# Performance work log

Measured on AMD Instinct MI355X. Metric: run time of the kernel, lower is better.

## Reference

```python
import jax, jax.numpy as jnp
import numpy as np
from jax import lax


def _conv(x, w, b):
    y = lax.conv_general_dilated(x, w, (1, 1), 'VALID',
                                 dimension_numbers=('NCHW', 'OIHW', 'NCHW'))
    return y + b[None, :, None, None]


def _cubic_weights(t):
    # torch bicubic kernel, A = -0.75
    A = -0.75
    def k1(u):
        return ((A + 2.0) * u - (A + 3.0)) * u * u + 1.0
    def k2(u):
        return ((A * u - 5.0 * A) * u + 8.0 * A) * u - 4.0 * A
    return (k2(t + 1.0), k1(t), k1(1.0 - t), k2(2.0 - t))


def _grid_sample_bicubic(img, grid):
    # img: (N,C,H,W); grid: (N,H,W,2) with (x,y) in [-1,1];
    # align_corners=False, padding_mode='zeros' (torch semantics)
    N, C, H, W = img.shape
    x = ((grid[..., 0] + 1.0) * W - 1.0) * 0.5
    y = ((grid[..., 1] + 1.0) * H - 1.0) * 0.5
    x0 = jnp.floor(x)
    y0 = jnp.floor(y)
    wx = _cubic_weights(x - x0)
    wy = _cubic_weights(y - y0)
    x0i = x0.astype(jnp.int32)
    y0i = y0.astype(jnp.int32)
    flat = img.reshape(N, C, H * W)
    Ho, Wo = x.shape[1], x.shape[2]
    out = jnp.zeros((N, C, Ho, Wo), img.dtype)
    for i in range(4):
        yi = y0i - 1 + i
        vy = (yi >= 0) & (yi < H)
        yic = jnp.clip(yi, 0, H - 1)
        for j in range(4):
            xj = x0i - 1 + j
            valid = vy & (xj >= 0) & (xj < W)
            xjc = jnp.clip(xj, 0, W - 1)
            idx = (yic * W + xjc).reshape(N, 1, Ho * Wo)
            v = jnp.take_along_axis(flat, idx, axis=2).reshape(N, C, Ho, Wo)
            w = jnp.where(valid, wy[i] * wx[j], 0.0)[:, None]
            out = out + v * w
    return out


def _warp_images(disp, images, novelLocation):
    # disp: (N,1,H,W); images: (N,20,H,W); novelLocation: (N,2,H,W)
    N, _, H, W = disp.shape
    d = jnp.moveaxis(disp, 1, -1)                      # (N,H,W,1)
    us = jnp.arange(H, dtype=jnp.float32)
    vs = jnp.arange(W, dtype=jnp.float32)
    gu, gv = jnp.meshgrid(us, vs, indexing='ij')       # torch default indexing
    base = jnp.stack((gu, gv), axis=-1)[None]          # (1,H,W,2) in (row,col)
    q = jnp.moveaxis(novelLocation, 1, -1)             # (N,H,W,2)
    scale = jnp.array([H - 1, W - 1], jnp.float32)
    warped = []
    for i in range(4):
        off = 5 * i
        img = images[:, off:off + 3]
        p = jnp.moveaxis(images[:, off + 3:off + 5], 1, -1)
        loc = base + (p - q) * d                       # (N,H,W,2) (row,col)
        loc = (loc / scale - 0.5) * 2.0
        loc = loc[..., ::-1]                           # flip -> (x=col, y=row)
        warped.append(_grid_sample_bicubic(img, loc))
    return jnp.concatenate(warped + [disp, novelLocation], axis=1)  # (N,15,H,W)


def _disparity_net(x, w1, b1, w2, b2, w3, b3, w4, b4):
    x = jax.nn.relu(_conv(x, w1, b1))
    x = jax.nn.relu(_conv(x, w2, b2))
    x = jax.nn.relu(_conv(x, w3, b3))
    return _conv(x, w4, b4)


def setup_inputs() -> dict:
    key = jax.random.key(0)
    ks = jax.random.split(key, 20)
    inp = {
        'disparityFeatures': jax.random.normal(ks[0], (4, 200, 268, 268), jnp.float32),
        'colorFeatures': jax.random.normal(ks[1], (4, 22, 256, 256), jnp.float32),
    }
    def conv_p(kw, kb, o, c, k):
        fan_in = c * k * k
        w = jax.random.normal(kw, (o, c, k, k), jnp.float32) / np.sqrt(fan_in)
        b = jax.random.normal(kb, (o,), jnp.float32) * 0.01
        return w, b
    inp['dw1'], inp['db1'] = conv_p(ks[2], ks[3], 100, 200, 7)
    inp['dw2'], inp['db2'] = conv_p(ks[4], ks[5], 100, 100, 5)
    inp['dw3'], inp['db3'] = conv_p(ks[6], ks[7], 50, 100, 3)
    inp['dw4'], inp['db4'] = conv_p(ks[8], ks[9], 1, 50, 1)
    inp['cw1'], inp['cb1'] = conv_p(ks[10], ks[11], 100, 15, 7)
    inp['cw2'], inp['cb2'] = conv_p(ks[12], ks[13], 100, 100, 5)
    inp['cw3'], inp['cb3'] = conv_p(ks[14], ks[15], 50, 100, 3)
    inp['cw4'], inp['cb4'] = conv_p(ks[16], ks[17], 3, 50, 1)
    return inp


def reference(disparityFeatures, colorFeatures,
              dw1, db1, dw2, db2, dw3, db3, dw4, db4,
              cw1, cb1, cw2, cb2, cw3, cb3, cw4, cb4):
    images = colorFeatures[:, :-2]
    novelLocation = colorFeatures[:, -2:]
    disparity = _disparity_net(disparityFeatures, dw1, db1, dw2, db2, dw3, db3, dw4, db4)
    warps = _warp_images(disparity, images, novelLocation)
    finalImg = _disparity_net(warps, cw1, cb1, cw2, cb2, cw3, cb3, cw4, cb4)
    return finalImg
```

## Files before the change

### kernel.cpp

```cpp
#include <hip/hip_runtime.h>
#include <cstddef>
#include <cstdint>

typedef _Float16 f16x8 __attribute__((ext_vector_type(8)));
typedef _Float16 f16x4 __attribute__((ext_vector_type(4)));
typedef float    f32x16 __attribute__((ext_vector_type(16)));

__global__ __launch_bounds__(256) void wtrans_kernel(
    const float* __restrict__ w, _Float16* __restrict__ Bt,
    int IC, int OC, int G, int K, int R, int ksteps)
{
    int gid = blockIdx.x * 256 + threadIdx.x;
    if (gid >= ksteps * G * 64) return;
    int ks   = gid / (G * 64);
    int rr   = gid - ks * G * 64;
    int g    = rr >> 6;
    int lane = rr & 63;
    int run = ks % R;
    int t2  = ks / R;
    int ky  = t2 % K;
    int chunk = t2 / K;
    int oc = g * 32 + (lane & 31);
    int kh = lane >> 5;
    _Float16 tmp[8];
    #pragma unroll
    for (int j = 0; j < 8; ++j) {
        int flat = run * 16 + kh * 8 + j;
        int xo  = flat / 20;
        int icl = flat - xo * 20;
        int ic  = chunk * 20 + icl;
        float v = 0.0f;
        if (oc < OC && ic < IC && xo < K)
            v = w[(((size_t)oc * IC + ic) * K + ky) * K + xo];
        tmp[j] = (_Float16)v;
    }
    *(uint4*)(Bt + (size_t)gid * 8) = *(uint4*)tmp;
}

__global__ __launch_bounds__(256) void convin_kernel(
    const float* __restrict__ src, _Float16* __restrict__ dst, int IC)
{
    constexpr int W = 268;
    constexpr int PADS = 272;
    __shared__ float s[20 * PADS];
    int y = blockIdx.x, chunk = blockIdx.y, img = blockIdx.z;
    int tid = threadIdx.x;
    for (int e = tid; e < 20 * W; e += 256) {
        int icl = e / W;
        int x = e - icl * W;
        int ic = chunk * 20 + icl;
        float v = 0.0f;
        if (ic < IC)
            v = src[(((size_t)img * IC + ic) * W + y) * W + x];
        s[icl * PADS + x] = v;
    }
    __syncthreads();
    _Float16* outRow = dst + ((size_t)(img * 10 + chunk) * W + y) * (W * 20);
    for (int u = tid; u < W * 20 / 8; u += 256) {
        _Float16 t[8];
        #pragma unroll
        for (int q = 0; q < 8; ++q) {
            int e = u * 8 + q;
            int px = e / 20;
            int c  = e - px * 20;
            t[q] = (_Float16)s[c * PADS + px];
        }
        *(uint4*)(outRow + (size_t)u * 8) = *(uint4*)t;
    }
}

template<int K, int WM, int WN, bool RELU>
__global__ __launch_bounds__(256, 2) void conv_mfma(
    const _Float16* __restrict__ in, const _Float16* __restrict__ Bt,
    const float* __restrict__ bias, _Float16* __restrict__ out,
    int Hin, int Win, int OC, int Ho, int Wo,
    int nchunks, int xb, int tilesPerImg,
    long inStride, long outStride)
{
    constexpr int CB = 20;
    constexpr int R  = (K * CB + 15) / 16;
    constexpr int BM = WM * 4;
    constexpr int PH = BM + K - 1;
    constexpr int MAXF = 31 * CB + R * 16;
    constexpr int PW = (((MAXF + CB - 1) / CB) + 1) & ~1;
    constexpr int ROWF = PW * CB;
    constexpr int UROW = ROWF / 8;
    constexpr int G    = WN * 2;
    constexpr int KSF  = G * 512;

    __shared__ __align__(16) _Float16 s[PH * ROWF];

    const int tid  = threadIdx.x;
    const int lane = tid & 63;
    const int wave = tid >> 6;
    const int wm   = (WN == 2) ? (wave & 1) : wave;
    const int wn   = (WN == 2) ? (wave >> 1) : 0;
    const int mcol = lane & 31;
    const int kh   = lane >> 5;
    const int alane = mcol * CB + kh * 8;

    int t = blockIdx.x;
    int img = t / tilesPerImg;
    int rem = t - img * tilesPerImg;
    int byi = rem / xb;
    int bxi = rem - byi * xb;
    int y0 = byi * BM; if (y0 > Ho - BM) y0 = Ho - BM;
    int x0 = bxi * 32; if (x0 > Wo - 32) x0 = Wo - 32;

    const _Float16* inI = in + (size_t)img * inStride;

    f32x16 acc[4][2];
    #pragma unroll
    for (int m = 0; m < 4; ++m)
        #pragma unroll
        for (int n = 0; n < 2; ++n)
            acc[m][n] = (f32x16)(0.0f);

    const int rowE = Win * CB;
    const int mxo  = rowE - 8;
    const size_t chStride = (size_t)Hin * rowE;

    #pragma unroll 1
    for (int chunk = 0; chunk < nchunks; ++chunk) {
        const _Float16* inC = inI + chunk * chStride + (size_t)y0 * rowE;
        #pragma unroll 1
        for (int e = tid; e < PH * UROW; e += 256) {
            int py = e / UROW;
            int uu = e - py * UROW;
            int off = x0 * CB + uu * 8;
            if (off > mxo) off = mxo;
            uint4 val = *(const uint4*)(inC + (size_t)py * rowE + off);
            *(uint4*)&s[(size_t)e * 8] = val;
        }
        __syncthreads();

        const _Float16* BtC = Bt + (size_t)(chunk * K) * R * KSF;
        #pragma unroll 1
        for (int ky = 0; ky < K; ++ky) {
            const _Float16* BtK = BtC + (size_t)(ky * R) * KSF;
            const int rbase = (wm * 4 + ky) * ROWF + alane;
            #pragma unroll
            for (int run = 0; run < R; ++run) {
                const _Float16* bp = BtK + (size_t)run * KSF + (wn * 128 + lane) * 8;
                f16x8 b0 = *(const f16x8*)bp;
                f16x8 b1 = *(const f16x8*)(bp + 512);
                const int ab = rbase + run * 16;
                #pragma unroll
                for (int mt = 0; mt < 4; ++mt) {
                    const _Float16* ap = &s[ab + mt * ROWF];
                    f16x4 lo = *(const f16x4*)ap;
                    f16x4 hi = *(const f16x4*)(ap + 4);
                    f16x8 a = __builtin_shufflevector(lo, hi, 0, 1, 2, 3, 4, 5, 6, 7);
                    acc[mt][0] = __builtin_amdgcn_mfma_f32_32x32x16_f16(a, b0, acc[mt][0], 0, 0, 0);
                    acc[mt][1] = __builtin_amdgcn_mfma_f32_32x32x16_f16(a, b1, acc[mt][1], 0, 0, 0);
                }
            }
        }
        __syncthreads();
    }

    _Float16* outI = out + (size_t)img * outStride;
    #pragma unroll
    for (int nt = 0; nt < 2; ++nt) {
        int oc = (wn * 2 + nt) * 32 + mcol;
        if (oc < OC) {
            float bv = bias[oc];
            int icc = oc / 20;
            int occ = oc - icc * 20;
            _Float16* base = outI + (size_t)icc * Ho * (Wo * 20) + occ;
            #pragma unroll
            for (int mt = 0; mt < 4; ++mt) {
                int y = y0 + wm * 4 + mt;
                _Float16* rowp = base + (size_t)y * (Wo * 20);
                #pragma unroll
                for (int reg = 0; reg < 16; ++reg) {
                    int x = x0 + (reg & 3) + 8 * (reg >> 2) + 4 * kh;
                    float v = acc[mt][nt][reg] + bv;
                    if (RELU) v = fmaxf(v, 0.0f);
                    rowp[(size_t)x * 20] = (_Float16)v;
                }
            }
        }
    }
}

template<int NOUT>
__global__ __launch_bounds__(256) void conv1x1_kernel(
    const _Float16* __restrict__ in, const float* __restrict__ w,
    const float* __restrict__ bias, float* __restrict__ out,
    int N, int IC, long inStride, long outStride)
{
    int px = blockIdx.x * 256 + threadIdx.x;
    int img = blockIdx.y;
    if (px >= N) return;
    const _Float16* p = in + (size_t)img * inStride;
    float a[NOUT];
    #pragma unroll
    for (int o = 0; o < NOUT; ++o) a[o] = 0.0f;
    for (int ic = 0; ic < IC; ++ic) {
        int icc = ic / 20;
        int icl = ic - icc * 20;
        float v = (float)p[((size_t)icc * N + px) * 20 + icl];
        #pragma unroll
        for (int o = 0; o < NOUT; ++o) a[o] = fmaf(v, w[o * IC + ic], a[o]);
    }
    #pragma unroll
    for (int o = 0; o < NOUT; ++o)
        out[(size_t)img * outStride + (size_t)o * N + px] = a[o] + bias[o];
}

__device__ __forceinline__ void cubicw(float t, float w[4])
{
    const float A = -0.75f;
    float u;
    u = t + 1.0f; w[0] = ((A * u - 5.0f * A) * u + 8.0f * A) * u - 4.0f * A;
    u = t;        w[1] = ((A + 2.0f) * u - (A + 3.0f)) * u * u + 1.0f;
    u = 1.0f - t; w[2] = ((A + 2.0f) * u - (A + 3.0f)) * u * u + 1.0f;
    u = 2.0f - t; w[3] = ((A * u - 5.0f * A) * u + 8.0f * A) * u - 4.0f * A;
}

__global__ __launch_bounds__(256) void warp_kernel(
    const float* __restrict__ disp, const float* __restrict__ cf,
    _Float16* __restrict__ outw)
{
    const int P = 65536;
    int idx = blockIdx.x * 256 + threadIdx.x;
    int img = blockIdx.y;
    const float* dI  = disp + (size_t)img * P;
    const float* cfI = cf + (size_t)img * 22 * P;
    _Float16* oI = outw + (size_t)img * 1310720 + (size_t)idx * 20;

    int u = idx >> 8;
    int v = idx & 255;

    float d  = dI[idx];
    float q0 = cfI[20 * P + idx];
    float q1 = cfI[21 * P + idx];

    for (int i = 0; i < 4; ++i) {
        const float* img5 = cfI + (size_t)(5 * i) * P;
        float p0 = img5[3 * P + idx];
        float p1 = img5[4 * P + idx];
        float lr = (float)u + (p0 - q0) * d;
        float lc = (float)v + (p1 - q1) * d;
        float gr = (lr / 255.0f - 0.5f) * 2.0f;
        float gc = (lc / 255.0f - 0.5f) * 2.0f;
        float x = ((gc + 1.0f) * 256.0f - 1.0f) * 0.5f;
        float y = ((gr + 1.0f) * 256.0f - 1.0f) * 0.5f;
        float xf = floorf(x), yf = floorf(y);
        float tx = x - xf, tyy = y - yf;
        float wx[4], wy[4];
        cubicw(tx, wx);
        cubicw(tyy, wy);
        int xi = (int)xf, yi = (int)yf;
        float a0 = 0.f, a1 = 0.f, a2 = 0.f;
        #pragma unroll
        for (int ii = 0; ii < 4; ++ii) {
            int yy = yi - 1 + ii;
            bool vy = (yy >= 0) && (yy < 256);
            int yc = min(max(yy, 0), 255);
            #pragma unroll
            for (int jj = 0; jj < 4; ++jj) {
                int xx = xi - 1 + jj;
                bool vv = vy && (xx >= 0) && (xx < 256);
                int xc = min(max(xx, 0), 255);
                float w = vv ? wy[ii] * wx[jj] : 0.0f;
                int pos = yc * 256 + xc;
                a0 = fmaf(img5[pos], w, a0);
                a1 = fmaf(img5[P + pos], w, a1);
                a2 = fmaf(img5[2 * P + pos], w, a2);
            }
        }
        oI[3 * i + 0] = (_Float16)a0;
        oI[3 * i + 1] = (_Float16)a1;
        oI[3 * i + 2] = (_Float16)a2;
    }
    oI[12] = (_Float16)d;
    oI[13] = (_Float16)q0;
    oI[14] = (_Float16)q1;
    #pragma unroll
    for (int c = 15; c < 20; ++c) oI[c] = (_Float16)0.0f;
}


extern "C" void kernel_launch(void* const* d_in, const int* in_sizes, int n_in,
                              void* d_out, int out_size, void* d_ws, size_t ws_size,
                              hipStream_t stream)
{
    const float* dF  = (const float*)d_in[0];
    const float* cF  = (const float*)d_in[1];
    const float* dw1 = (const float*)d_in[2];
    const float* db1 = (const float*)d_in[3];
    const float* dw2 = (const float*)d_in[4];
    const float* db2 = (const float*)d_in[5];
    const float* dw3 = (const float*)d_in[6];
    const float* db3 = (const float*)d_in[7];
    const float* dw4 = (const float*)d_in[8];
    const float* db4 = (const float*)d_in[9];
    const float* cw1 = (const float*)d_in[10];
    const float* cb1 = (const float*)d_in[11];
    const float* cw2 = (const float*)d_in[12];
    const float* cb2 = (const float*)d_in[13];
    const float* cw3 = (const float*)d_in[14];
    const float* cb3 = (const float*)d_in[15];
    const float* cw4 = (const float*)d_in[16];
    const float* cb4 = (const float*)d_in[17];

    float* outp = (float*)d_out;
    char* ws = (char*)d_ws;

    const size_t O_D1 = 0;
    const size_t O_D2 = O_D1 + 2580480;
    const size_t O_D3 = O_D2 + 716800;
    const size_t O_C1 = O_D3 + 122880;
    const size_t O_C2 = O_C1 + 258048;
    const size_t O_C3 = O_C2 + 716800;
    const size_t O_WEND = O_C3 + 122880;

    _Float16* bt_d1 = (_Float16*)(ws + O_D1);
    _Float16* bt_d2 = (_Float16*)(ws + O_D2);
    _Float16* bt_d3 = (_Float16*)(ws + O_D3);
    _Float16* bt_c1 = (_Float16*)(ws + O_C1);
    _Float16* bt_c2 = (_Float16*)(ws + O_C2);
    _Float16* bt_c3 = (_Float16*)(ws + O_C3);

    auto T = [&](const float* w, _Float16* bt, int IC, int OC, int G,
                 int K, int R, int ksteps) {
        int n = ksteps * G * 64;
        wtrans_kernel<<<(n + 255) / 256, 256, 0, stream>>>(w, bt, IC, OC, G, K, R, ksteps);
    };
    T(dw1, bt_d1, 200, 100, 4, 7, 9, 630);
    T(dw2, bt_d2, 100, 100, 4, 5, 7, 175);
    T(dw3, bt_d3, 100,  50, 2, 3, 4,  60);
    T(cw1, bt_c1,  15, 100, 4, 7, 9,  63);
    T(cw2, bt_c2, 100, 100, 4, 5, 7, 175);
    T(cw3, bt_c3, 100,  50, 2, 3, 4,  60);

    const size_t PER_IMG = (14364800ull + 6864400ull + 6656400ull) * 2;
    int batch = (ws_size >= O_WEND + 4ull * PER_IMG + 1024) ? 4
              : (ws_size >= O_WEND + 2ull * PER_IMG + 1024) ? 2 : 1;

    for (int g0 = 0; g0 < 4; g0 += batch) {
        const int N = batch;
        char* base = ws + O_WEND;
        _Float16* dFc  = (_Float16*)base;
        _Float16* bufA = (_Float16*)(base + 28729600ull * N);
        _Float16* bufB = (_Float16*)(base + (28729600ull + 13728800ull) * N);
        _Float16* bufC = (_Float16*)base;
        float*    disp = (float*)(base + 7864320ull * N);
        _Float16* wrp  = (_Float16*)(base + (7864320ull + 262144ull) * N);

        const float* dFg = dF + (size_t)g0 * 200 * 268 * 268;
        const float* cFg = cF + (size_t)g0 * 22 * 65536;
        float* outg = outp + (size_t)g0 * 3 * 59536;

        convin_kernel<<<dim3(268, 10, N), 256, 0, stream>>>(dFg, dFc, 200);

        conv_mfma<7, 2, 2, true><<<9 * 33 * N, 256, 0, stream>>>(
            dFc, bt_d1, db1, bufA, 268, 268, 100, 262, 262, 10, 9, 9 * 33,
            14364800L, 6864400L);
        conv_mfma<5, 2, 2, true><<<9 * 33 * N, 256, 0, stream>>>(
            bufA, bt_d2, db2, bufB, 262, 262, 100, 258, 258, 5, 9, 9 * 33,
            6864400L, 6656400L);
        conv_mfma<3, 4, 1, true><<<8 * 16 * N, 256, 0, stream>>>(
            bufB, bt_d3, db3, bufC, 258, 258, 50, 256, 256, 5, 8, 8 * 16,
            6656400L, 3932160L);
        conv1x1_kernel<1><<<dim3(256, N), 256, 0, stream>>>(
            bufC, dw4, db4, disp, 65536, 50, 3932160L, 65536L);

        warp_kernel<<<dim3(256, N), 256, 0, stream>>>(disp, cFg, wrp);

        conv_mfma<7, 2, 2, true><<<8 * 32 * N, 256, 0, stream>>>(
            wrp, bt_c1, cb1, bufA, 256, 256, 100, 250, 250, 1, 8, 8 * 32,
            1310720L, 6250000L);
        conv_mfma<5, 2, 2, true><<<8 * 31 * N, 256, 0, stream>>>(
            bufA, bt_c2, cb2, bufB, 250, 250, 100, 246, 246, 5, 8, 8 * 31,
            6250000L, 6051600L);
        conv_mfma<3, 4, 1, true><<<8 * 16 * N, 256, 0, stream>>>(
            bufB, bt_c3, cb3, bufC, 246, 246, 50, 244, 244, 5, 8, 8 * 16,
            6051600L, 3932160L);
        conv1x1_kernel<3><<<dim3(233, N), 256, 0, stream>>>(
            bufC, cw4, cb4, outg, 59536, 50, 3932160L, 178608L);
    }
}
```

Baseline: 1.811 ms.

## Double-buffer conv input tiles in LDS using async global_load_lds prefetch

The conv MFMA kernel now stages each input-channel chunk into one of two LDS buffers with direct global-to-LDS loads. It prefetches the next chunk while MFMAs run on the current one, which removes the load-then-barrier stall at the top of every chunk. It also raises wave priority around the MFMA inner block. The cost is double the LDS footprint, which may limit occupancy. Correctness depends on the barrier waiting for the async LDS writes to finish.

```diff
diff --git a/kernel.cpp b/kernel.cpp
--- a/kernel.cpp
+++ b/kernel.cpp
@@ -85,10 +85,12 @@
     constexpr int PW = (((MAXF + CB - 1) / CB) + 1) & ~1;
     constexpr int ROWF = PW * CB;
     constexpr int UROW = ROWF / 8;
+    constexpr int TOT  = PH * UROW;
     constexpr int G    = WN * 2;
     constexpr int KSF  = G * 512;
-
-    __shared__ __align__(16) _Float16 s[PH * ROWF];
+    constexpr int BUF  = PH * ROWF;
+
+    __shared__ __align__(16) _Float16 s[2 * BUF];
 
     const int tid  = threadIdx.x;
     const int lane = tid & 63;
@@ -120,20 +122,35 @@
     const int mxo  = rowE - 8;
     const size_t chStride = (size_t)Hin * rowE;
 
+    auto stage = [&](int chunk, int which) {
+        const _Float16* inC = inI + chunk * chStride + (size_t)y0 * rowE;
+        #pragma unroll
+        for (int it = 0; it < (TOT + 255) / 256; ++it) {
+            int e = it * 256 + tid;
+            if (e < TOT) {
+                int py = e / UROW;
+                int uu = e - py * UROW;
+                int off = x0 * CB + uu * 8;
+                if (off > mxo) off = mxo;
+                const _Float16* src = inC + (size_t)py * rowE + off;
+                _Float16* dst = s + (size_t)which * BUF
+                                  + (size_t)(it * 256 + (tid & ~63)) * 8;
+                __builtin_amdgcn_global_load_lds(
+                    (const __attribute__((address_space(1))) void*)src,
+                    (__attribute__((address_space(3))) void*)dst, 16, 0, 0);
+            }
+        }
+    };
+
+    stage(0, 0);
+    __syncthreads();
+    int cur = 0;
+
     #pragma unroll 1
     for (int chunk = 0; chunk < nchunks; ++chunk) {
-        const _Float16* inC = inI + chunk * chStride + (size_t)y0 * rowE;
-        #pragma unroll 1
-        for (int e = tid; e < PH * UROW; e += 256) {
-            int py = e / UROW;
-            int uu = e - py * UROW;
-            int off = x0 * CB + uu * 8;
-            if (off > mxo) off = mxo;
-            uint4 val = *(const uint4*)(inC + (size_t)py * rowE + off);
-            *(uint4*)&s[(size_t)e * 8] = val;
-        }
-        __syncthreads();
-
+        if (chunk + 1 < nchunks) stage(chunk + 1, cur ^ 1);
+
+        const _Float16* sb = s + (size_t)cur * BUF;
         const _Float16* BtC = Bt + (size_t)(chunk * K) * R * KSF;
         #pragma unroll 1
         for (int ky = 0; ky < K; ++ky) {
@@ -145,18 +162,23 @@
                 f16x8 b0 = *(const f16x8*)bp;
                 f16x8 b1 = *(const f16x8*)(bp + 512);
                 const int ab = rbase + run * 16;
+                __builtin_amdgcn_s_setprio(1);
                 #pragma unroll
                 for (int mt = 0; mt < 4; ++mt) {
-                    const _Float16* ap = &s[ab + mt * ROWF];
+                    const _Float16* ap = &sb[ab + mt * ROWF];
                     f16x4 lo = *(const f16x4*)ap;
                     f16x4 hi = *(const f16x4*)(ap + 4);
                     f16x8 a = __builtin_shufflevector(lo, hi, 0, 1, 2, 3, 4, 5, 6, 7);
                     acc[mt][0] = __builtin_amdgcn_mfma_f32_32x32x16_f16(a, b0, acc[mt][0], 0, 0, 0);
                     acc[mt][1] = __builtin_amdgcn_mfma_f32_32x32x16_f16(a, b1, acc[mt][1], 0, 0, 0);
                 }
+                __builtin_amdgcn_s_setprio(0);
             }
         }
-        __syncthreads();
+        if (chunk + 1 < nchunks) {
+            __syncthreads();
+            cur ^= 1;
+        }
     }
 
     _Float16* outI = out + (size_t)img * outStride;
```

Measured after the change: 1.929 ms. +6.6%, slower.

## Shrink conv tiles to 8 rows and split output-channel groups across blocks

Applied to the files above, without the earlier changes.

The MFMA conv kernel now uses a fixed 8-row tile with each wave handling 2 rows. Output-channel groups are split across separate blocks through a new OG parameter, where before waves inside one block split them. This doubles the grid size and cuts accumulator registers, and launch bounds are raised to 3 blocks per CU to improve occupancy and load balance. In exchange, each block reloads the input halo for its own channel group, so halo and input loads from global memory are duplicated.

```diff
diff --git a/kernel.cpp b/kernel.cpp
--- a/kernel.cpp
+++ b/kernel.cpp
@@ -69,32 +69,29 @@
     }
 }
 
-template<int K, int WM, int WN, bool RELU>
-__global__ __launch_bounds__(256, 2) void conv_mfma(
+template<int K, bool RELU>
+__global__ __launch_bounds__(256, 3) void conv_mfma(
     const _Float16* __restrict__ in, const _Float16* __restrict__ Bt,
     const float* __restrict__ bias, _Float16* __restrict__ out,
     int Hin, int Win, int OC, int Ho, int Wo,
-    int nchunks, int xb, int tilesPerImg,
+    int nchunks, int xb, int tilesPerImg, int OG,
     long inStride, long outStride)
 {
     constexpr int CB = 20;
     constexpr int R  = (K * CB + 15) / 16;
-    constexpr int BM = WM * 4;
+    constexpr int BM = 8;
     constexpr int PH = BM + K - 1;
     constexpr int MAXF = 31 * CB + R * 16;
     constexpr int PW = (((MAXF + CB - 1) / CB) + 1) & ~1;
     constexpr int ROWF = PW * CB;
     constexpr int UROW = ROWF / 8;
-    constexpr int G    = WN * 2;
-    constexpr int KSF  = G * 512;
+    constexpr int TOT  = PH * UROW;
 
     __shared__ __align__(16) _Float16 s[PH * ROWF];
 
     const int tid  = threadIdx.x;
     const int lane = tid & 63;
-    const int wave = tid >> 6;
-    const int wm   = (WN == 2) ? (wave & 1) : wave;
-    const int wn   = (WN == 2) ? (wave >> 1) : 0;
+    const int wm   = tid >> 6;
     const int mcol = lane & 31;
     const int kh   = lane >> 5;
     const int alane = mcol * CB + kh * 8;
@@ -102,16 +99,20 @@
     int t = blockIdx.x;
     int img = t / tilesPerImg;
     int rem = t - img * tilesPerImg;
-    int byi = rem / xb;
-    int bxi = rem - byi * xb;
+    int og  = rem % OG;
+    int tile = rem / OG;
+    int byi = tile / xb;
+    int bxi = tile - byi * xb;
     int y0 = byi * BM; if (y0 > Ho - BM) y0 = Ho - BM;
     int x0 = bxi * 32; if (x0 > Wo - 32) x0 = Wo - 32;
 
+    const int KSF = OG * 1024;
+
     const _Float16* inI = in + (size_t)img * inStride;
 
-    f32x16 acc[4][2];
-    #pragma unroll
-    for (int m = 0; m < 4; ++m)
+    f32x16 acc[2][2];
+    #pragma unroll
+    for (int m = 0; m < 2; ++m)
         #pragma unroll
         for (int n = 0; n < 2; ++n)
             acc[m][n] = (f32x16)(0.0f);
@@ -124,7 +125,7 @@
     for (int chunk = 0; chunk < nchunks; ++chunk) {
         const _Float16* inC = inI + chunk * chStride + (size_t)y0 * rowE;
         #pragma unroll 1
-        for (int e = tid; e < PH * UROW; e += 256) {
+        for (int e = tid; e < TOT; e += 256) {
             int py = e / UROW;
             int uu = e - py * UROW;
             int off = x0 * CB + uu * 8;
@@ -138,15 +139,15 @@
         #pragma unroll 1
         for (int ky = 0; ky < K; ++ky) {
             const _Float16* BtK = BtC + (size_t)(ky * R) * KSF;
-            const int rbase = (wm * 4 + ky) * ROWF + alane;
+            const int rbase = (wm * 2 + ky) * ROWF + alane;
             #pragma unroll
             for (int run = 0; run < R; ++run) {
-                const _Float16* bp = BtK + (size_t)run * KSF + (wn * 128 + lane) * 8;
+                const _Float16* bp = BtK + (size_t)run * KSF + og * 1024 + lane * 8;
                 f16x8 b0 = *(const f16x8*)bp;
                 f16x8 b1 = *(const f16x8*)(bp + 512);
                 const int ab = rbase + run * 16;
                 #pragma unroll
-                for (int mt = 0; mt < 4; ++mt) {
+                for (int mt = 0; mt < 2; ++mt) {
                     const _Float16* ap = &s[ab + mt * ROWF];
                     f16x4 lo = *(const f16x4*)ap;
                     f16x4 hi = *(const f16x4*)(ap + 4);
@@ -162,15 +163,15 @@
     _Float16* outI = out + (size_t)img * outStride;
     #pragma unroll
     for (int nt = 0; nt < 2; ++nt) {
-        int oc = (wn * 2 + nt) * 32 + mcol;
+        int oc = (og * 2 + nt) * 32 + mcol;
         if (oc < OC) {
             float bv = bias[oc];
             int icc = oc / 20;
             int occ = oc - icc * 20;
             _Float16* base = outI + (size_t)icc * Ho * (Wo * 20) + occ;
             #pragma unroll
-            for (int mt = 0; mt < 4; ++mt) {
-                int y = y0 + wm * 4 + mt;
+            for (int mt = 0; mt < 2; ++mt) {
+                int y = y0 + wm * 2 + mt;
                 _Float16* rowp = base + (size_t)y * (Wo * 20);
                 #pragma unroll
                 for (int reg = 0; reg < 16; ++reg) {
@@ -356,28 +357,28 @@
 
         convin_kernel<<<dim3(268, 10, N), 256, 0, stream>>>(dFg, dFc, 200);
 
-        conv_mfma<7, 2, 2, true><<<9 * 33 * N, 256, 0, stream>>>(
-            dFc, bt_d1, db1, bufA, 268, 268, 100, 262, 262, 10, 9, 9 * 33,
+        conv_mfma<7, true><<<594 * N, 256, 0, stream>>>(
+            dFc, bt_d1, db1, bufA, 268, 268, 100, 262, 262, 10, 9, 594, 2,
             14364800L, 6864400L);
-        conv_mfma<5, 2, 2, true><<<9 * 33 * N, 256, 0, stream>>>(
-            bufA, bt_d2, db2, bufB, 262, 262, 100, 258, 258, 5, 9, 9 * 33,
+        conv_mfma<5, true><<<594 * N, 256, 0, stream>>>(
+            bufA, bt_d2, db2, bufB, 262, 262, 100, 258, 258, 5, 9, 594, 2,
             6864400L, 6656400L);
-        conv_mfma<3, 4, 1, true><<<8 * 16 * N, 256, 0, stream>>>(
-            bufB, bt_d3, db3, bufC, 258, 258, 50, 256, 256, 5, 8, 8 * 16,
+        conv_mfma<3, true><<<256 * N, 256, 0, stream>>>(
+            bufB, bt_d3, db3, bufC, 258, 258, 50, 256, 256, 5, 8, 256, 1,
             6656400L, 3932160L);
         conv1x1_kernel<1><<<dim3(256, N), 256, 0, stream>>>(
             bufC, dw4, db4, disp, 65536, 50, 3932160L, 65536L);
 
         warp_kernel<<<dim3(256, N), 256, 0, stream>>>(disp, cFg, wrp);
 
-        conv_mfma<7, 2, 2, true><<<8 * 32 * N, 256, 0, stream>>>(
-            wrp, bt_c1, cb1, bufA, 256, 256, 100, 250, 250, 1, 8, 8 * 32,
+        conv_mfma<7, true><<<512 * N, 256, 0, stream>>>(
+            wrp, bt_c1, cb1, bufA, 256, 256, 100, 250, 250, 1, 8, 512, 2,
             1310720L, 6250000L);
-        conv_mfma<5, 2, 2, true><<<8 * 31 * N, 256, 0, stream>>>(
-            bufA, bt_c2, cb2, bufB, 250, 250, 100, 246, 246, 5, 8, 8 * 31,
+        conv_mfma<5, true><<<496 * N, 256, 0, stream>>>(
+            bufA, bt_c2, cb2, bufB, 250, 250, 100, 246, 246, 5, 8, 496, 2,
             6250000L, 6051600L);
-        conv_mfma<3, 4, 1, true><<<8 * 16 * N, 256, 0, stream>>>(
-            bufB, bt_c3, cb3, bufC, 246, 246, 50, 244, 244, 5, 8, 8 * 16,
+        conv_mfma<3, true><<<248 * N, 256, 0, stream>>>(
+            bufB, bt_c3, cb3, bufC, 246, 246, 50, 244, 244, 5, 8, 248, 1,
             6051600L, 3932160L);
         conv1x1_kernel<3><<<dim3(233, N), 256, 0, stream>>>(
             bufC, cw4, cb4, outg, 59536, 50, 3932160L, 178608L);
```

After: 1.905 ms. 5.2% more time.
